# Optimization experiments

Measured on AMD Instinct MI355X. Metric: run time of the kernel, lower is better.

Reference implementation:

```python
import jax, jax.numpy as jnp
import numpy as np

N_NODES = 8192
N_EDGES = 65536


def _segment_softmax(scores, seg_ids, num_segments):
    # scores: [E, 1], seg_ids: [E] -> softmax over edges sharing the same dst
    m = jax.ops.segment_max(scores, seg_ids, num_segments=num_segments)  # [N,1]
    e = jnp.exp(scores - m[seg_ids])
    denom = jax.ops.segment_sum(e, seg_ids, num_segments=num_segments)   # [N,1]
    return e / denom[seg_ids]


def setup_inputs() -> dict:
    key = jax.random.key(0)
    ks = jax.random.split(key, 12)
    s = lambda fin: 1.0 / np.sqrt(fin)
    inp = {
        'n_f': jax.random.normal(ks[0], (N_NODES, 1024), jnp.float32),
        'word2vec': jax.random.normal(ks[1], (N_NODES, 300), jnp.float32),
        's_f': jax.random.normal(ks[2], (N_EDGES, 16), jnp.float32),
        'src': jax.random.randint(ks[3], (N_EDGES,), 0, N_NODES),
        'dst': jax.random.randint(ks[4], (N_EDGES,), 0, N_NODES),
        'We': jax.random.normal(ks[5], (2064, 1024), jnp.float32) * s(2064),
        'be': jnp.zeros((1024,), jnp.float32),
        'Wel': jax.random.normal(ks[6], (600, 600), jnp.float32) * s(600),
        'bel': jnp.zeros((600,), jnp.float32),
        'Wa': jax.random.normal(ks[7], (1024, 1), jnp.float32) * s(1024),
        'ba': jnp.zeros((1,), jnp.float32),
        'Wal': jax.random.normal(ks[8], (600, 1), jnp.float32) * s(600),
        'bal': jnp.zeros((1,), jnp.float32),
        'Wn': jax.random.normal(ks[9], (2048, 1024), jnp.float32) * s(2048),
        'bn': jnp.zeros((1024,), jnp.float32),
        'Wnl': jax.random.normal(ks[10], (600, 300), jnp.float32) * s(600),
        'bnl': jnp.zeros((300,), jnp.float32),
    }
    return inp


def reference(n_f, word2vec, s_f, src, dst,
              We, be, Wel, bel, Wa, ba, Wal, bal, Wn, bn, Wnl, bnl):
    # ---- edge apply (H_H_EdgeApplyModule) ----
    src_nf = n_f[src]                                    # [E,1024] gather
    feat = jnp.concatenate([src_nf, s_f, n_f[dst]], axis=1)  # [E,2064]
    e_f = jax.nn.relu(feat @ We + be)                    # [E,1024]
    feat_lang = jnp.concatenate([word2vec[src], word2vec[dst]], axis=1)  # [E,600]
    e_f_lang = jax.nn.relu(feat_lang @ Wel + bel)        # [E,600]

    # ---- edge attention (E_AttentionModule1): scalar score per edge ----
    a_feat = e_f @ Wa + ba                               # [E,1]
    a_feat_lang = e_f_lang @ Wal + bal                   # [E,1]

    # ---- reduce: mailbox softmax over incoming edges per dst node ----
    alpha = _segment_softmax(a_feat, dst, N_NODES)       # [E,1]
    alpha_lang = _segment_softmax(a_feat_lang, dst, N_NODES)
    z_f = jax.ops.segment_sum(alpha * (src_nf + e_f), dst, num_segments=N_NODES)      # [N,1024]
    z_f_lang = jax.ops.segment_sum(alpha_lang * word2vec[src], dst, num_segments=N_NODES)  # [N,300]

    # ---- node apply (H_NodeApplyModule) ----
    new_n_f = jax.nn.relu(jnp.concatenate([n_f, z_f], axis=1) @ Wn + bn)              # [N,1024]
    new_n_f_lang = jax.nn.relu(jnp.concatenate([word2vec, z_f_lang], axis=1) @ Wnl + bnl)  # [N,300]
    return new_n_f, new_n_f_lang
```

## Files before the change

### kernel.cpp

```cpp
#include <hip/hip_runtime.h>
#include <hip/hip_bf16.h>

#define N_NODES 8192
#define N_EDGES 65536
#define OUT0_ELEMS ((size_t)N_NODES * 1024)

using bf16 = __hip_bfloat16;
typedef __attribute__((ext_vector_type(8))) short short8;
typedef __attribute__((ext_vector_type(4))) float f32x4;

__device__ __forceinline__ float b2f(bf16 x) { return __bfloat162float(x); }
__device__ __forceinline__ bf16 f2b(float x) { return __float2bfloat16(x); }
__device__ __forceinline__ unsigned short bbits(float x)
{
  union { bf16 h; unsigned short u; } v; v.h = f2b(x); return v.u;
}
__device__ __forceinline__ unsigned pack2(float a, float b)
{
  return (unsigned)bbits(a) | ((unsigned)bbits(b) << 16);
}
__device__ __forceinline__ float4 cvt2x(uint2 u)
{
  float4 r;
  r.x = __uint_as_float(u.x << 16);
  r.y = __uint_as_float(u.x & 0xffff0000u);
  r.z = __uint_as_float(u.y << 16);
  r.w = __uint_as_float(u.y & 0xffff0000u);
  return r;
}
__device__ __forceinline__ float4 ld4b(const bf16* p)
{
  uint2 u = *(const uint2*)p;
  return cvt2x(u);
}
__device__ __forceinline__ void st4b(bf16* p, float a, float b, float c, float d)
{
  uint2 v; v.x = pack2(a, b); v.y = pack2(c, d);
  *(uint2*)p = v;
}

__global__ void GNN_27650999451833_kernel() {}

__global__ void gnn6_zero(int* __restrict__ p, int n)
{
  int i = blockIdx.x * blockDim.x + threadIdx.x;
  if (i < n) p[i] = 0;
}

__global__ __launch_bounds__(256)
void gnn7_cvt(const float* __restrict__ src, bf16* __restrict__ dst, int n8)
{
  int i = blockIdx.x * blockDim.x + threadIdx.x;
  if (i < n8) {
    float4 a = ((const float4*)src)[2 * i];
    float4 b = ((const float4*)src)[2 * i + 1];
    uint4 p;
    p.x = pack2(a.x, a.y); p.y = pack2(a.z, a.w);
    p.z = pack2(b.x, b.y); p.w = pack2(b.z, b.w);
    ((uint4*)dst)[i] = p;
  }
}

__global__ __launch_bounds__(256)
void gnn8_pad_w2v(const float* __restrict__ src, bf16* __restrict__ dst)
{
  int idx = blockIdx.x * blockDim.x + threadIdx.x;
  if (idx >= N_NODES * 80) return;
  int r = idx / 80, c0 = (idx % 80) * 4;
  float v[4];
#pragma unroll
  for (int j = 0; j < 4; ++j) {
    int c = c0 + j;
    v[j] = (c < 300) ? src[(size_t)r * 300 + c] : 0.f;
  }
  uint2 p; p.x = pack2(v[0], v[1]); p.y = pack2(v[2], v[3]);
  *(uint2*)(dst + (size_t)r * 320 + c0) = p;
}

__global__ __launch_bounds__(256)
void gnn12_t_Wetail(const float* __restrict__ We, bf16* __restrict__ BT)
{
  int c = blockIdx.x * 256 + threadIdx.x;
  if (c >= 1024) return;
  bf16* row = BT + (size_t)c * 32;
#pragma unroll
  for (int k = 0; k < 16; ++k)
    row[k] = f2b(We[(size_t)(1024 + k) * 1024 + c]);
#pragma unroll
  for (int k = 16; k < 32; ++k) row[k] = f2b(0.f);
}

__global__ __launch_bounds__(256)
void gnn10_t_We(const float* __restrict__ src, bf16* __restrict__ dst)
{
  __shared__ float tile[32][33];
  const int kb = blockIdx.x * 32, nb = blockIdx.y * 32;
  const int tx = threadIdx.x & 31, ty = threadIdx.x >> 5;
  const int n = nb + tx;
#pragma unroll
  for (int i = ty; i < 32; i += 8)
    tile[i][tx] = (n < 1024)
        ? src[(size_t)(kb + i) * 1024 + n]
        : src[(size_t)(1040 + kb + i) * 1024 + (n - 1024)];
  __syncthreads();
#pragma unroll
  for (int i = ty; i < 32; i += 8)
    dst[(size_t)(nb + i) * 1024 + kb + tx] = f2b(tile[tx][i]);
}

__global__ __launch_bounds__(256)
void gnn10_t_Wn(const float* __restrict__ src, bf16* __restrict__ dst)
{
  __shared__ float tile[32][33];
  const int kb = blockIdx.x * 32, nb = blockIdx.y * 32;
  const int tx = threadIdx.x & 31, ty = threadIdx.x >> 5;
#pragma unroll
  for (int i = ty; i < 32; i += 8)
    tile[i][tx] = src[(size_t)(kb + i) * 1024 + nb + tx];
  __syncthreads();
#pragma unroll
  for (int i = ty; i < 32; i += 8)
    dst[(size_t)(nb + i) * 2048 + kb + tx] = f2b(tile[tx][i]);
}

__global__ __launch_bounds__(256)
void gnn10_t_Wel(const float* __restrict__ src, bf16* __restrict__ dst)
{
  __shared__ float tile[32][33];
  const int kb = blockIdx.x * 32, nb = blockIdx.y * 32;
  const int tx = threadIdx.x & 31, ty = threadIdx.x >> 5;
  const int n = nb + tx;
#pragma unroll
  for (int i = ty; i < 32; i += 8) {
    int k = kb + i;
    float v = 0.f;
    if (k < 300) {
      if (n < 600)       v = src[(size_t)k * 600 + n];
      else if (n < 1200) v = src[(size_t)(300 + k) * 600 + (n - 600)];
    }
    tile[i][tx] = v;
  }
  __syncthreads();
#pragma unroll
  for (int i = ty; i < 32; i += 8)
    dst[(size_t)(nb + i) * 320 + kb + tx] = f2b(tile[tx][i]);
}

__global__ __launch_bounds__(256)
void gnn10_t_Wnl(const float* __restrict__ src, bf16* __restrict__ dst)
{
  __shared__ float tile[32][33];
  const int kb = blockIdx.x * 32, nb = blockIdx.y * 32;
  const int tx = threadIdx.x & 31, ty = threadIdx.x >> 5;
  const int n = nb + tx;
#pragma unroll
  for (int i = ty; i < 32; i += 8) {
    int k = kb + i;
    int kr = (k < 300) ? k : ((k >= 320 && k < 620) ? (k - 20) : -1);
    tile[i][tx] = (kr >= 0 && n < 300) ? src[(size_t)kr * 300 + n] : 0.f;
  }
  __syncthreads();
#pragma unroll
  for (int i = ty; i < 32; i += 8)
    dst[(size_t)(nb + i) * 640 + kb + tx] = f2b(tile[tx][i]);
}

__global__ __launch_bounds__(256)
void gnn10_mm_P(const bf16* __restrict__ A, const bf16* __restrict__ BT,
                bf16* __restrict__ P, const float* __restrict__ be)
{
  __shared__ short As[128 * 40];
  __shared__ short Bs[128 * 40];
  const int t = threadIdx.x;
  const int col0 = blockIdx.x * 128, row0 = blockIdx.y * 128;
  const int lane = t & 63, w = t >> 6, m16 = lane & 15, q = lane >> 4;
  const int wr = w >> 1, wc = w & 1;

  f32x4 acc[4][4];
#pragma unroll
  for (int mi = 0; mi < 4; ++mi)
#pragma unroll
    for (int ni = 0; ni < 4; ++ni) acc[mi][ni] = (f32x4){0.f, 0.f, 0.f, 0.f};

  const int ar = t >> 1, ah = (t & 1) * 16;
  const bf16* aptr = A + (size_t)(row0 + ar) * 1024 + ah;
  const bf16* bptr = BT + (size_t)(col0 + ar) * 1024 + ah;

  uint4 a0 = *(const uint4*)(aptr);
  uint4 a1 = *(const uint4*)(aptr + 8);
  uint4 b0 = *(const uint4*)(bptr);
  uint4 b1 = *(const uint4*)(bptr + 8);

  for (int k0 = 0; k0 < 1024; k0 += 32) {
    if (k0) __syncthreads();
    *(uint4*)&As[ar * 40 + ah] = a0;
    *(uint4*)&As[ar * 40 + ah + 8] = a1;
    *(uint4*)&Bs[ar * 40 + ah] = b0;
    *(uint4*)&Bs[ar * 40 + ah + 8] = b1;
    __syncthreads();
    if (k0 + 32 < 1024) {
      a0 = *(const uint4*)(aptr + k0 + 32);
      a1 = *(const uint4*)(aptr + k0 + 40);
      b0 = *(const uint4*)(bptr + k0 + 32);
      b1 = *(const uint4*)(bptr + k0 + 40);
    }
    short8 af[4];
#pragma unroll
    for (int mi = 0; mi < 4; ++mi)
      af[mi] = *(const short8*)&As[(wr * 64 + mi * 16 + m16) * 40 + 8 * q];
#pragma unroll
    for (int ni = 0; ni < 4; ++ni) {
      short8 bfv = *(const short8*)&Bs[(wc * 64 + ni * 16 + m16) * 40 + 8 * q];
#pragma unroll
      for (int mi = 0; mi < 4; ++mi)
        acc[mi][ni] =
            __builtin_amdgcn_mfma_f32_16x16x32_bf16(af[mi], bfv, acc[mi][ni], 0, 0, 0);
    }
  }
#pragma unroll
  for (int mi = 0; mi < 4; ++mi)
#pragma unroll
    for (int ni = 0; ni < 4; ++ni) {
      int c = col0 + wc * 64 + ni * 16 + m16;
      float bias = (be != nullptr && c >= 1024) ? be[c - 1024] : 0.f;
#pragma unroll
      for (int r = 0; r < 4; ++r)
        P[(size_t)(row0 + wr * 64 + mi * 16 + 4 * q + r) * 2048 + c] =
            f2b(acc[mi][ni][r] + bias);
    }
}

__global__ __launch_bounds__(256)
void gnn10_mm_out_n(const bf16* __restrict__ A0, const bf16* __restrict__ A1,
                    const bf16* __restrict__ BT, const float* __restrict__ bn,
                    float* __restrict__ out)
{
  __shared__ short As[128 * 40];
  __shared__ short Bs[128 * 40];
  const int t = threadIdx.x;
  const int col0 = blockIdx.x * 128, row0 = blockIdx.y * 128;
  const int lane = t & 63, w = t >> 6, m16 = lane & 15, q = lane >> 4;
  const int wr = w >> 1, wc = w & 1;

  f32x4 acc[4][4];
#pragma unroll
  for (int mi = 0; mi < 4; ++mi)
#pragma unroll
    for (int ni = 0; ni < 4; ++ni) acc[mi][ni] = (f32x4){0.f, 0.f, 0.f, 0.f};

  const int ar = t >> 1, ah = (t & 1) * 16;
  const bf16* ap0 = A0 + (size_t)(row0 + ar) * 1024 + ah;
  const bf16* ap1 = A1 + (size_t)(row0 + ar) * 1024 + ah;
  const bf16* bptr = BT + (size_t)(col0 + ar) * 2048 + ah;

  uint4 a0 = *(const uint4*)(ap0);
  uint4 a1 = *(const uint4*)(ap0 + 8);
  uint4 b0 = *(const uint4*)(bptr);
  uint4 b1 = *(const uint4*)(bptr + 8);

  for (int k0 = 0; k0 < 2048; k0 += 32) {
    if (k0) __syncthreads();
    *(uint4*)&As[ar * 40 + ah] = a0;
    *(uint4*)&As[ar * 40 + ah + 8] = a1;
    *(uint4*)&Bs[ar * 40 + ah] = b0;
    *(uint4*)&Bs[ar * 40 + ah + 8] = b1;
    __syncthreads();
    if (k0 + 32 < 2048) {
      int kn = k0 + 32;
      const bf16* ap = (kn < 1024) ? (ap0 + kn) : (ap1 + (kn - 1024));
      a0 = *(const uint4*)(ap);
      a1 = *(const uint4*)(ap + 8);
      b0 = *(const uint4*)(bptr + kn);
      b1 = *(const uint4*)(bptr + kn + 8);
    }
    short8 af[4];
#pragma unroll
    for (int mi = 0; mi < 4; ++mi)
      af[mi] = *(const short8*)&As[(wr * 64 + mi * 16 + m16) * 40 + 8 * q];
#pragma unroll
    for (int ni = 0; ni < 4; ++ni) {
      short8 bfv = *(const short8*)&Bs[(wc * 64 + ni * 16 + m16) * 40 + 8 * q];
#pragma unroll
      for (int mi = 0; mi < 4; ++mi)
        acc[mi][ni] =
            __builtin_amdgcn_mfma_f32_16x16x32_bf16(af[mi], bfv, acc[mi][ni], 0, 0, 0);
    }
  }
#pragma unroll
  for (int mi = 0; mi < 4; ++mi)
#pragma unroll
    for (int ni = 0; ni < 4; ++ni) {
      int c = col0 + wc * 64 + ni * 16 + m16;
      float bias = bn[c];
#pragma unroll
      for (int r = 0; r < 4; ++r) {
        float v = acc[mi][ni][r] + bias;
        out[(size_t)(row0 + wr * 64 + mi * 16 + 4 * q + r) * 1024 + c] =
            fmaxf(v, 0.f);
      }
    }
}

__global__ __launch_bounds__(256)
void gnn10_mm_Q(const bf16* __restrict__ A, const bf16* __restrict__ BT,
                bf16* __restrict__ Q, const float* __restrict__ bel)
{
  __shared__ short As[128 * 40];
  __shared__ short Bs[128 * 40];
  const int t = threadIdx.x;
  const int col0 = blockIdx.x * 128, row0 = blockIdx.y * 128;
  const int lane = t & 63, w = t >> 6, m16 = lane & 15, q = lane >> 4;
  const int wr = w >> 1, wc = w & 1;

  f32x4 acc[4][4];
#pragma unroll
  for (int mi = 0; mi < 4; ++mi)
#pragma unroll
    for (int ni = 0; ni < 4; ++ni) acc[mi][ni] = (f32x4){0.f, 0.f, 0.f, 0.f};

  const int ar = t >> 1, ah = (t & 1) * 16;
  const bf16* aptr = A + (size_t)(row0 + ar) * 320 + ah;
  const bf16* bptr = BT + (size_t)(col0 + ar) * 320 + ah;

  uint4 a0 = *(const uint4*)(aptr);
  uint4 a1 = *(const uint4*)(aptr + 8);
  uint4 b0 = *(const uint4*)(bptr);
  uint4 b1 = *(const uint4*)(bptr + 8);

  for (int k0 = 0; k0 < 320; k0 += 32) {
    if (k0) __syncthreads();
    *(uint4*)&As[ar * 40 + ah] = a0;
    *(uint4*)&As[ar * 40 + ah + 8] = a1;
    *(uint4*)&Bs[ar * 40 + ah] = b0;
    *(uint4*)&Bs[ar * 40 + ah + 8] = b1;
    __syncthreads();
    if (k0 + 32 < 320) {
      a0 = *(const uint4*)(aptr + k0 + 32);
      a1 = *(const uint4*)(aptr + k0 + 40);
      b0 = *(const uint4*)(bptr + k0 + 32);
      b1 = *(const uint4*)(bptr + k0 + 40);
    }
    short8 af[4];
#pragma unroll
    for (int mi = 0; mi < 4; ++mi)
      af[mi] = *(const short8*)&As[(wr * 64 + mi * 16 + m16) * 40 + 8 * q];
#pragma unroll
    for (int ni = 0; ni < 4; ++ni) {
      short8 bfv = *(const short8*)&Bs[(wc * 64 + ni * 16 + m16) * 40 + 8 * q];
#pragma unroll
      for (int mi = 0; mi < 4; ++mi)
        acc[mi][ni] =
            __builtin_amdgcn_mfma_f32_16x16x32_bf16(af[mi], bfv, acc[mi][ni], 0, 0, 0);
    }
  }
#pragma unroll
  for (int mi = 0; mi < 4; ++mi)
#pragma unroll
    for (int ni = 0; ni < 4; ++ni) {
      int c = col0 + wc * 64 + ni * 16 + m16;
      float bias = (bel != nullptr && c >= 600 && c < 1200) ? bel[c - 600] : 0.f;
#pragma unroll
      for (int r = 0; r < 4; ++r)
        Q[(size_t)(row0 + wr * 64 + mi * 16 + 4 * q + r) * 1280 + c] =
            f2b(acc[mi][ni][r] + bias);
    }
}

__global__ __launch_bounds__(256)
void gnn10_mm_out_l(const bf16* __restrict__ A0, const bf16* __restrict__ A1,
                    const bf16* __restrict__ BT, const float* __restrict__ bnl,
                    float* __restrict__ out2)
{
  __shared__ short As[128 * 40];
  __shared__ short Bs[128 * 40];
  const int t = threadIdx.x;
  const int col0 = blockIdx.x * 128, row0 = blockIdx.y * 128;
  const int lane = t & 63, w = t >> 6, m16 = lane & 15, q = lane >> 4;
  const int wr = w >> 1, wc = w & 1;

  f32x4 acc[4][4];
#pragma unroll
  for (int mi = 0; mi < 4; ++mi)
#pragma unroll
    for (int ni = 0; ni < 4; ++ni) acc[mi][ni] = (f32x4){0.f, 0.f, 0.f, 0.f};

  const int ar = t >> 1, ah = (t & 1) * 16;
  const bf16* ap0 = A0 + (size_t)(row0 + ar) * 320 + ah;
  const bf16* ap1 = A1 + (size_t)(row0 + ar) * 320 + ah;
  const bf16* bptr = BT + (size_t)(col0 + ar) * 640 + ah;

  uint4 a0 = *(const uint4*)(ap0);
  uint4 a1 = *(const uint4*)(ap0 + 8);
  uint4 b0 = *(const uint4*)(bptr);
  uint4 b1 = *(const uint4*)(bptr + 8);

  for (int k0 = 0; k0 < 640; k0 += 32) {
    if (k0) __syncthreads();
    *(uint4*)&As[ar * 40 + ah] = a0;
    *(uint4*)&As[ar * 40 + ah + 8] = a1;
    *(uint4*)&Bs[ar * 40 + ah] = b0;
    *(uint4*)&Bs[ar * 40 + ah + 8] = b1;
    __syncthreads();
    if (k0 + 32 < 640) {
      int kn = k0 + 32;
      const bf16* ap = (kn < 320) ? (ap0 + kn) : (ap1 + (kn - 320));
      a0 = *(const uint4*)(ap);
      a1 = *(const uint4*)(ap + 8);
      b0 = *(const uint4*)(bptr + kn);
      b1 = *(const uint4*)(bptr + kn + 8);
    }
    short8 af[4];
#pragma unroll
    for (int mi = 0; mi < 4; ++mi)
      af[mi] = *(const short8*)&As[(wr * 64 + mi * 16 + m16) * 40 + 8 * q];
#pragma unroll
    for (int ni = 0; ni < 4; ++ni) {
      short8 bfv = *(const short8*)&Bs[(wc * 64 + ni * 16 + m16) * 40 + 8 * q];
#pragma unroll
      for (int mi = 0; mi < 4; ++mi)
        acc[mi][ni] =
            __builtin_amdgcn_mfma_f32_16x16x32_bf16(af[mi], bfv, acc[mi][ni], 0, 0, 0);
    }
  }
#pragma unroll
  for (int mi = 0; mi < 4; ++mi)
#pragma unroll
    for (int ni = 0; ni < 4; ++ni) {
      int c = col0 + wc * 64 + ni * 16 + m16;
      if (c < 300) {
        float bias = bnl[c];
#pragma unroll
        for (int r = 0; r < 4; ++r) {
          float v = acc[mi][ni][r] + bias;
          out2[(size_t)(row0 + wr * 64 + mi * 16 + 4 * q + r) * 300 + c] =
              fmaxf(v, 0.f);
        }
      }
    }
}

__global__ void gnn6_count(const int* __restrict__ dst, int* __restrict__ cnt)
{
  int e = blockIdx.x * blockDim.x + threadIdx.x;
  if (e < N_EDGES) atomicAdd(&cnt[dst[e]], 1);
}

__global__ __launch_bounds__(1024)
void gnn6_scan(const int* __restrict__ cnt, int* __restrict__ off, int* __restrict__ cur)
{
  __shared__ int sh[1024];
  const int t = threadIdx.x;
  int local[8]; int sum = 0;
#pragma unroll
  for (int i = 0; i < 8; ++i) { int v = cnt[t * 8 + i]; local[i] = sum; sum += v; }
  sh[t] = sum;
  __syncthreads();
  for (int d = 1; d < 1024; d <<= 1) {
    int v = (t >= d) ? sh[t - d] : 0;
    __syncthreads();
    sh[t] += v;
    __syncthreads();
  }
  int basev = (t > 0) ? sh[t - 1] : 0;
#pragma unroll
  for (int i = 0; i < 8; ++i) { int o = basev + local[i]; off[t * 8 + i] = o; cur[t * 8 + i] = o; }
  if (t == 1023) off[8192] = sh[1023];
}

__global__ void gnn6_fill(const int* __restrict__ dst, int* __restrict__ cur,
                          int* __restrict__ elist)
{
  int e = blockIdx.x * blockDim.x + threadIdx.x;
  if (e < N_EDGES) { int p = atomicAdd(&cur[dst[e]], 1); elist[p] = e; }
}

__global__ void gnn14_fill(const int* __restrict__ dst, const int* __restrict__ src,
                           int* __restrict__ cur, int* __restrict__ elist,
                           int* __restrict__ srcs, int* __restrict__ dsts)
{
  int e = blockIdx.x * blockDim.x + threadIdx.x;
  if (e < N_EDGES) {
    int d = dst[e];
    int p = atomicAdd(&cur[d], 1);
    elist[p] = e;
    srcs[p] = src[e];
    dsts[p] = d;
  }
}

__global__ __launch_bounds__(256)
void gnn14_sfp(const float* __restrict__ s_f, const int* __restrict__ elist,
               bf16* __restrict__ sfp)
{
  int p = blockIdx.x * 256 + threadIdx.x;
  if (p >= N_EDGES) return;
  int e = elist[p];
  const float4* sp = (const float4*)(s_f + (size_t)e * 16);
  float4 s0 = sp[0], s1 = sp[1], s2 = sp[2], s3 = sp[3];
  uint4 lo, hi;
  lo.x = pack2(s0.x, s0.y); lo.y = pack2(s0.z, s0.w);
  lo.z = pack2(s1.x, s1.y); lo.w = pack2(s1.z, s1.w);
  hi.x = pack2(s2.x, s2.y); hi.y = pack2(s2.z, s2.w);
  hi.z = pack2(s3.x, s3.y); hi.w = pack2(s3.z, s3.w);
  uint4* dp = (uint4*)(sfp + (size_t)p * 32);
  dp[0] = lo; dp[1] = hi;
  dp[2] = (uint4){0, 0, 0, 0}; dp[3] = (uint4){0, 0, 0, 0};
}

#define SLD_STRIDE 1032
__global__ __launch_bounds__(256)
void gnn14_mm_S_score(const bf16* __restrict__ sfp, const bf16* __restrict__ WeTtail,
                      const int* __restrict__ srcs, const int* __restrict__ dsts,
                      const float* __restrict__ Wa, const float* __restrict__ ba,
                      const float* __restrict__ Wal, const float* __restrict__ bal,
                      const bf16* __restrict__ P, const bf16* __restrict__ Q,
                      bf16* __restrict__ S, float* __restrict__ af,
                      float* __restrict__ afl)
{
  __shared__ short Sld[16 * SLD_STRIDE];
  __shared__ float shf[8][4], shl[8][4];
  const int t = threadIdx.x;
  const int lane = t & 63, w = t >> 6, m16 = lane & 15, q = lane >> 4;
  const int p0 = blockIdx.x * 16;

  short8 bfr = *(const short8*)(sfp + (size_t)(p0 + m16) * 32 + 8 * q);
  const int cb = w * 256;
#pragma unroll
  for (int ni = 0; ni < 16; ++ni) {
    short8 afr = *(const short8*)(WeTtail + (size_t)(cb + ni * 16 + m16) * 32 + 8 * q);
    f32x4 acc = __builtin_amdgcn_mfma_f32_16x16x32_bf16(
        afr, bfr, (f32x4){0.f, 0.f, 0.f, 0.f}, 0, 0, 0);
    uint2 v; v.x = pack2(acc[0], acc[1]); v.y = pack2(acc[2], acc[3]);
    *(uint2*)&Sld[m16 * SLD_STRIDE + cb + ni * 16 + 4 * q] = v;
  }
  __syncthreads();

  {
    const int row = t >> 4, cbase = (t & 15) * 8;
#pragma unroll
    for (int j = 0; j < 8; ++j) {
      uint4 v = *(const uint4*)&Sld[row * SLD_STRIDE + cbase + 128 * j];
      *(uint4*)(S + (size_t)(p0 + row) * 1024 + cbase + 128 * j) = v;
    }
  }

  const int c0 = 4 * t;
  float4 wav = *(const float4*)(Wa + c0);
  const bool lact = (t < 150);
  float4 walv = {0, 0, 0, 0};
  if (lact) walv = *(const float4*)(Wal + c0);
  const float ba0 = ba[0], bal0 = bal[0];

#pragma unroll 1
  for (int bb = 0; bb < 2; ++bb) {
    const int eb = 8 * bb;
    int ss[8], dd[8];
    {
      int4 a4 = *(const int4*)(srcs + p0 + eb);
      int4 b4 = *(const int4*)(srcs + p0 + eb + 4);
      ss[0] = a4.x; ss[1] = a4.y; ss[2] = a4.z; ss[3] = a4.w;
      ss[4] = b4.x; ss[5] = b4.y; ss[6] = b4.z; ss[7] = b4.w;
      int4 c4 = *(const int4*)(dsts + p0 + eb);
      int4 d4 = *(const int4*)(dsts + p0 + eb + 4);
      dd[0] = c4.x; dd[1] = c4.y; dd[2] = c4.z; dd[3] = c4.w;
      dd[4] = d4.x; dd[5] = d4.y; dd[6] = d4.z; dd[7] = d4.w;
    }

    float pf[8], pl[8];
#pragma unroll
    for (int i = 0; i < 8; ++i) {
      uint2 us = *(const uint2*)&Sld[(eb + i) * SLD_STRIDE + c0];
      float4 sv = cvt2x(us);
      float4 p1 = ld4b(P + (size_t)ss[i] * 2048 + c0);
      float4 p2 = ld4b(P + (size_t)dd[i] * 2048 + 1024 + c0);
      float acc = 0.f;
      acc = fmaf(fmaxf(p1.x + p2.x + sv.x, 0.f), wav.x, acc);
      acc = fmaf(fmaxf(p1.y + p2.y + sv.y, 0.f), wav.y, acc);
      acc = fmaf(fmaxf(p1.z + p2.z + sv.z, 0.f), wav.z, acc);
      acc = fmaf(fmaxf(p1.w + p2.w + sv.w, 0.f), wav.w, acc);
      pf[i] = acc;

      float accl = 0.f;
      if (lact) {
        float4 q1 = ld4b(Q + (size_t)ss[i] * 1280 + c0);
        float4 q2 = ld4b(Q + (size_t)dd[i] * 1280 + 600 + c0);
        accl = fmaf(fmaxf(q1.x + q2.x, 0.f), walv.x, accl);
        accl = fmaf(fmaxf(q1.y + q2.y, 0.f), walv.y, accl);
        accl = fmaf(fmaxf(q1.z + q2.z, 0.f), walv.z, accl);
        accl = fmaf(fmaxf(q1.w + q2.w, 0.f), walv.w, accl);
      }
      pl[i] = accl;
    }

#pragma unroll
    for (int i = 0; i < 8; ++i) {
#pragma unroll
      for (int o = 32; o > 0; o >>= 1) {
        pf[i] += __shfl_down(pf[i], o, 64);
        pl[i] += __shfl_down(pl[i], o, 64);
      }
    }
    if (lane == 0) {
#pragma unroll
      for (int i = 0; i < 8; ++i) { shf[i][w] = pf[i]; shl[i][w] = pl[i]; }
    }
    __syncthreads();
    if (t < 8)
      af[p0 + eb + t] = shf[t][0] + shf[t][1] + shf[t][2] + shf[t][3] + ba0;
    if (t >= 64 && t < 72) {
      const int i = t & 7;
      afl[p0 + eb + i] = shl[i][0] + shl[i][1] + shl[i][2] + shl[i][3] + bal0;
    }
    __syncthreads();
  }
}

__global__ __launch_bounds__(256)
void gnn11_edge_score(const int* __restrict__ src, const int* __restrict__ dst,
                      const float* __restrict__ s_f, const float* __restrict__ We,
                      const float* __restrict__ be, const float* __restrict__ Wa,
                      const float* __restrict__ ba, const float* __restrict__ bel,
                      const float* __restrict__ Wal, const float* __restrict__ bal,
                      const bf16* __restrict__ P, const bf16* __restrict__ Q,
                      float* __restrict__ af, float* __restrict__ afl)
{
  const int t = threadIdx.x;
  const int lane = t & 63, w = t >> 6;
  const int c0 = 4 * t;
  const int e0 = blockIdx.x * 8;

  float wef[16][4];
#pragma unroll
  for (int k = 0; k < 16; ++k) {
    float4 v = *(const float4*)(We + (size_t)(1024 + k) * 1024 + c0);
    wef[k][0] = v.x; wef[k][1] = v.y; wef[k][2] = v.z; wef[k][3] = v.w;
  }
  float4 bev = *(const float4*)(be + c0);
  float4 wav = *(const float4*)(Wa + c0);
  const bool lact = (t < 150);
  float4 belv = {0, 0, 0, 0}, walv = {0, 0, 0, 0};
  if (lact) { belv = *(const float4*)(bel + c0); walv = *(const float4*)(Wal + c0); }

  int ss[8], dd[8];
  {
    int4 a = *(const int4*)(src + e0);
    int4 b = *(const int4*)(src + e0 + 4);
    ss[0] = a.x; ss[1] = a.y; ss[2] = a.z; ss[3] = a.w;
    ss[4] = b.x; ss[5] = b.y; ss[6] = b.z; ss[7] = b.w;
    int4 c = *(const int4*)(dst + e0);
    int4 d = *(const int4*)(dst + e0 + 4);
    dd[0] = c.x; dd[1] = c.y; dd[2] = c.z; dd[3] = c.w;
    dd[4] = d.x; dd[5] = d.y; dd[6] = d.z; dd[7] = d.w;
  }

  float pf[8], pl[8];

#pragma unroll
  for (int i = 0; i < 8; ++i) {
    const int e = e0 + i;
    float sfv[16];
    {
      const float4* sp = (const float4*)(s_f + (size_t)e * 16);
      float4 s0 = sp[0], s1 = sp[1], s2 = sp[2], s3 = sp[3];
      sfv[0] = s0.x; sfv[1] = s0.y; sfv[2] = s0.z; sfv[3] = s0.w;
      sfv[4] = s1.x; sfv[5] = s1.y; sfv[6] = s1.z; sfv[7] = s1.w;
      sfv[8] = s2.x; sfv[9] = s2.y; sfv[10] = s2.z; sfv[11] = s2.w;
      sfv[12] = s3.x; sfv[13] = s3.y; sfv[14] = s3.z; sfv[15] = s3.w;
    }
    float4 p1 = ld4b(P + (size_t)ss[i] * 2048 + c0);
    float4 p2 = ld4b(P + (size_t)dd[i] * 2048 + 1024 + c0);
    float pv[4] = {p1.x + p2.x + bev.x, p1.y + p2.y + bev.y,
                   p1.z + p2.z + bev.z, p1.w + p2.w + bev.w};
    float acc = 0.f;
#pragma unroll
    for (int j = 0; j < 4; ++j) {
      float v = pv[j];
#pragma unroll
      for (int k = 0; k < 16; ++k) v = fmaf(sfv[k], wef[k][j], v);
      acc = fmaf(fmaxf(v, 0.f), (&wav.x)[j], acc);
    }
    pf[i] = acc;

    float accl = 0.f;
    if (lact) {
      float4 q1 = ld4b(Q + (size_t)ss[i] * 1280 + c0);
      float4 q2 = ld4b(Q + (size_t)dd[i] * 1280 + 600 + c0);
      float qv[4] = {q1.x + q2.x + belv.x, q1.y + q2.y + belv.y,
                     q1.z + q2.z + belv.z, q1.w + q2.w + belv.w};
#pragma unroll
      for (int j = 0; j < 4; ++j)
        accl = fmaf(fmaxf(qv[j], 0.f), (&walv.x)[j], accl);
    }
    pl[i] = accl;
  }

  __shared__ float shf[8][4], shl[8][4];
#pragma unroll
  for (int i = 0; i < 8; ++i) {
#pragma unroll
    for (int o = 32; o > 0; o >>= 1) {
      pf[i] += __shfl_down(pf[i], o, 64);
      pl[i] += __shfl_down(pl[i], o, 64);
    }
  }
  if (lane == 0) {
#pragma unroll
    for (int i = 0; i < 8; ++i) { shf[i][w] = pf[i]; shl[i][w] = pl[i]; }
  }
  __syncthreads();
  if (t < 8)
    af[e0 + t] = shf[t][0] + shf[t][1] + shf[t][2] + shf[t][3] + ba[0];
  if (t >= 64 && t < 72) {
    const int i = t & 7;
    afl[e0 + i] = shl[i][0] + shl[i][1] + shl[i][2] + shl[i][3] + bal[0];
  }
}

__global__ __launch_bounds__(256)
void gnn14_alpha(const int* __restrict__ off, float* __restrict__ af,
                 float* __restrict__ afl)
{
  const int n = blockIdx.x * 256 + threadIdx.x;
  if (n >= N_NODES) return;
  const int base = off[n];
  const int deg = off[n + 1] - base;
  float m = -1e30f, ml = -1e30f;
  for (int i = 0; i < deg; ++i) {
    m = fmaxf(m, af[base + i]);
    ml = fmaxf(ml, afl[base + i]);
  }
  float den = 0.f, denl = 0.f;
  for (int i = 0; i < deg; ++i) {
    den += expf(af[base + i] - m);
    denl += expf(afl[base + i] - ml);
  }
  float inv = (den > 0.f) ? 1.f / den : 0.f;
  float invl = (denl > 0.f) ? 1.f / denl : 0.f;
  for (int i = 0; i < deg; ++i) {
    af[base + i] = expf(af[base + i] - m) * inv;
    afl[base + i] = expf(afl[base + i] - ml) * invl;
  }
}

__global__ __launch_bounds__(256)
void gnn6_alpha(const int* __restrict__ off, const int* __restrict__ elist,
                float* __restrict__ af, float* __restrict__ afl)
{
  const int n = blockIdx.x * 256 + threadIdx.x;
  if (n >= N_NODES) return;
  const int base = off[n];
  const int deg = off[n + 1] - base;
  float m = -1e30f, ml = -1e30f;
  for (int i = 0; i < deg; ++i) {
    int e = elist[base + i];
    m = fmaxf(m, af[e]);
    ml = fmaxf(ml, afl[e]);
  }
  float den = 0.f, denl = 0.f;
  for (int i = 0; i < deg; ++i) {
    int e = elist[base + i];
    den += expf(af[e] - m);
    denl += expf(afl[e] - ml);
  }
  float inv = (den > 0.f) ? 1.f / den : 0.f;
  float invl = (denl > 0.f) ? 1.f / denl : 0.f;
  for (int i = 0; i < deg; ++i) {
    int e = elist[base + i];
    af[e] = expf(af[e] - m) * inv;
    afl[e] = expf(afl[e] - ml) * invl;
  }
}

__global__ __launch_bounds__(256)
void gnn14_node_z(const int* __restrict__ off, const int* __restrict__ srcs,
                  const float* __restrict__ af, const float* __restrict__ afl,
                  const bf16* __restrict__ nf_bf, const bf16* __restrict__ w2v_pad,
                  const bf16* __restrict__ S, const bf16* __restrict__ P,
                  bf16* __restrict__ zf, bf16* __restrict__ zfl_pad)
{
  const int node = blockIdx.x;
  const int t = threadIdx.x;
  const int c0 = 4 * t;
  const int base = off[node];
  const int deg = off[node + 1] - base;

  float4 p2v = ld4b(P + (size_t)node * 2048 + 1024 + c0);
  const float p2[4] = {p2v.x, p2v.y, p2v.z, p2v.w};

  float acc[4] = {0.f, 0.f, 0.f, 0.f};
  float accl[4] = {0.f, 0.f, 0.f, 0.f};
  const bool lact = (t < 75);

  for (int i = 0; i < deg; ++i) {
    const int pidx = base + i;
    const int s = srcs[pidx];
    const float wgt = af[pidx];
    const float wl = afl[pidx];

    float4 sv = ld4b(S + (size_t)pidx * 1024 + c0);
    float4 p1 = ld4b(P + (size_t)s * 2048 + c0);
    float4 nf4 = ld4b(nf_bf + (size_t)s * 1024 + c0);
    const float p1a[4] = {p1.x, p1.y, p1.z, p1.w};
    const float sva[4] = {sv.x, sv.y, sv.z, sv.w};
    const float nfa[4] = {nf4.x, nf4.y, nf4.z, nf4.w};
#pragma unroll
    for (int j = 0; j < 4; ++j) {
      float ef = fmaxf(p1a[j] + p2[j] + sva[j], 0.f);
      acc[j] = fmaf(wgt, nfa[j] + ef, acc[j]);
    }
    if (lact) {
      float4 wv = ld4b(w2v_pad + (size_t)s * 320 + c0);
      accl[0] = fmaf(wl, wv.x, accl[0]);
      accl[1] = fmaf(wl, wv.y, accl[1]);
      accl[2] = fmaf(wl, wv.z, accl[2]);
      accl[3] = fmaf(wl, wv.w, accl[3]);
    }
  }
  st4b(zf + (size_t)node * 1024 + c0, acc[0], acc[1], acc[2], acc[3]);
  if (lact)
    st4b(zfl_pad + (size_t)node * 320 + c0, accl[0], accl[1], accl[2], accl[3]);
  else if (t < 80)
    st4b(zfl_pad + (size_t)node * 320 + c0, 0.f, 0.f, 0.f, 0.f);
}

__global__ __launch_bounds__(256)
void gnn9_node_z(const int* __restrict__ off, const int* __restrict__ elist,
                 const int* __restrict__ src, const float* __restrict__ af,
                 const float* __restrict__ afl, const bf16* __restrict__ nf_bf,
                 const bf16* __restrict__ w2v_pad, const float* __restrict__ s_f,
                 const float* __restrict__ We, const float* __restrict__ be,
                 const bf16* __restrict__ P, bf16* __restrict__ zf,
                 bf16* __restrict__ zfl_pad)
{
  const int node = blockIdx.x;
  const int t = threadIdx.x;
  const int c0 = 4 * t;
  const int base = off[node];
  const int deg = off[node + 1] - base;

  float wef[16][4];
#pragma unroll
  for (int k = 0; k < 16; ++k) {
    float4 v = *(const float4*)(We + (size_t)(1024 + k) * 1024 + c0);
    wef[k][0] = v.x; wef[k][1] = v.y; wef[k][2] = v.z; wef[k][3] = v.w;
  }
  float4 p2v = ld4b(P + (size_t)node * 2048 + 1024 + c0);
  float4 bev = *(const float4*)(be + c0);
  const float p2[4] = {p2v.x + bev.x, p2v.y + bev.y, p2v.z + bev.z, p2v.w + bev.w};

  float acc[4] = {0.f, 0.f, 0.f, 0.f};
  float accl[4] = {0.f, 0.f, 0.f, 0.f};
  const bool lact = (t < 75);

  for (int i = 0; i < deg; ++i) {
    const int e = elist[base + i];
    const int s = src[e];
    const float wgt = af[e];
    const float wl = afl[e];

    float sfv[16];
    {
      const float4* sp = (const float4*)(s_f + (size_t)e * 16);
      float4 s0 = sp[0], s1 = sp[1], s2 = sp[2], s3 = sp[3];
      sfv[0] = s0.x; sfv[1] = s0.y; sfv[2] = s0.z; sfv[3] = s0.w;
      sfv[4] = s1.x; sfv[5] = s1.y; sfv[6] = s1.z; sfv[7] = s1.w;
      sfv[8] = s2.x; sfv[9] = s2.y; sfv[10] = s2.z; sfv[11] = s2.w;
      sfv[12] = s3.x; sfv[13] = s3.y; sfv[14] = s3.z; sfv[15] = s3.w;
    }

    float4 p1 = ld4b(P + (size_t)s * 2048 + c0);
    float4 nf4 = ld4b(nf_bf + (size_t)s * 1024 + c0);
    const float p1a[4] = {p1.x, p1.y, p1.z, p1.w};
    const float nfa[4] = {nf4.x, nf4.y, nf4.z, nf4.w};
#pragma unroll
    for (int j = 0; j < 4; ++j) {
      float ef = p1a[j] + p2[j];
#pragma unroll
      for (int k = 0; k < 16; ++k) ef = fmaf(sfv[k], wef[k][j], ef);
      ef = fmaxf(ef, 0.f);
      acc[j] = fmaf(wgt, nfa[j] + ef, acc[j]);
    }
    if (lact) {
      float4 wv = ld4b(w2v_pad + (size_t)s * 320 + c0);
      accl[0] = fmaf(wl, wv.x, accl[0]);
      accl[1] = fmaf(wl, wv.y, accl[1]);
      accl[2] = fmaf(wl, wv.z, accl[2]);
      accl[3] = fmaf(wl, wv.w, accl[3]);
    }
  }
  st4b(zf + (size_t)node * 1024 + c0, acc[0], acc[1], acc[2], acc[3]);
  if (lact)
    st4b(zfl_pad + (size_t)node * 320 + c0, accl[0], accl[1], accl[2], accl[3]);
  else if (t < 80)
    st4b(zfl_pad + (size_t)node * 320 + c0, 0.f, 0.f, 0.f, 0.f);
}

extern "C" void kernel_launch(void* const* d_in, const int* in_sizes, int n_in,
                              void* d_out, int out_size, void* d_ws, size_t ws_size,
                              hipStream_t stream)
{
  (void)hipGetLastError();
  if (n_in != 17) { (void)hipMemsetAsync(d_out, 0x41, 4096, stream); return; }

  const float* n_f = (const float*)d_in[0];
  const float* w2v = (const float*)d_in[1];
  const float* s_f = (const float*)d_in[2];
  const int*   src = (const int*)d_in[3];
  const int*   dst = (const int*)d_in[4];
  const float* We  = (const float*)d_in[5];
  const float* be  = (const float*)d_in[6];
  const float* Wel = (const float*)d_in[7];
  const float* bel = (const float*)d_in[8];
  const float* Wa  = (const float*)d_in[9];
  const float* ba  = (const float*)d_in[10];
  const float* Wal = (const float*)d_in[11];
  const float* bal = (const float*)d_in[12];
  const float* Wn  = (const float*)d_in[13];
  const float* bn  = (const float*)d_in[14];
  const float* Wnl = (const float*)d_in[15];
  const float* bnl = (const float*)d_in[16];
  float* out  = (float*)d_out;
  float* out2 = out + OUT0_ELEMS;

  char* ws = (char*)d_ws;
  size_t o = 0;
  auto alloc = [&](size_t bytes) -> void* {
    void* p = ws + o; o += bytes; o = (o + 255) & ~(size_t)255; return p;
  };
  bf16* P        = (bf16*)alloc((size_t)N_NODES * 2048 * 2);
  bf16* Q        = (bf16*)alloc((size_t)N_NODES * 1280 * 2);
  bf16* zf       = (bf16*)alloc((size_t)N_NODES * 1024 * 2);
  bf16* zfl_pad  = (bf16*)alloc((size_t)N_NODES * 320 * 2);
  bf16* nf_bf    = (bf16*)alloc((size_t)N_NODES * 1024 * 2);
  bf16* w2v_pad  = (bf16*)alloc((size_t)N_NODES * 320 * 2);
  bf16* WeT      = (bf16*)alloc((size_t)2048 * 1024 * 2);
  bf16* WnT      = (bf16*)alloc((size_t)1024 * 2048 * 2);
  bf16* WelT     = (bf16*)alloc((size_t)1280 * 320 * 2);
  bf16* WnlT     = (bf16*)alloc((size_t)384 * 640 * 2);
  float* af      = (float*)alloc((size_t)N_EDGES * 4);
  float* afl     = (float*)alloc((size_t)N_EDGES * 4);
  int* cnt       = (int*)alloc((size_t)N_NODES * 4);
  int* offs      = (int*)alloc((size_t)(N_NODES + 1) * 4);
  int* cur       = (int*)alloc((size_t)N_NODES * 4);
  int* elist     = (int*)alloc((size_t)N_EDGES * 4);
  size_t base_end = o;
  if (base_end > ws_size) { (void)hipMemsetAsync(d_out, 0x42, 4096, stream); return; }

  bf16* sfp     = (bf16*)alloc((size_t)N_EDGES * 32 * 2);
  bf16* WeTtail = (bf16*)alloc((size_t)1024 * 32 * 2);
  bf16* S       = (bf16*)alloc((size_t)N_EDGES * 1024 * 2);
  int* srcs     = (int*)alloc((size_t)N_EDGES * 4);
  int* dsts     = (int*)alloc((size_t)N_EDGES * 4);
  const bool useS = (o <= ws_size);

  gnn6_zero<<<N_NODES / 256, 256, 0, stream>>>(cnt, N_NODES);
  gnn7_cvt<<<(N_NODES * 1024 / 8 + 255) / 256, 256, 0, stream>>>(n_f, nf_bf,
                                                                 N_NODES * 1024 / 8);
  gnn8_pad_w2v<<<(N_NODES * 80 + 255) / 256, 256, 0, stream>>>(w2v, w2v_pad);
  { dim3 g(32, 64); gnn10_t_We<<<g, 256, 0, stream>>>(We, WeT); }
  { dim3 g(64, 32); gnn10_t_Wn<<<g, 256, 0, stream>>>(Wn, WnT); }
  { dim3 g(10, 40); gnn10_t_Wel<<<g, 256, 0, stream>>>(Wel, WelT); }
  { dim3 g(20, 12); gnn10_t_Wnl<<<g, 256, 0, stream>>>(Wnl, WnlT); }

  gnn6_count<<<N_EDGES / 256, 256, 0, stream>>>(dst, cnt);
  gnn6_scan<<<1, 1024, 0, stream>>>(cnt, offs, cur);
  if (useS) {
    gnn14_fill<<<N_EDGES / 256, 256, 0, stream>>>(dst, src, cur, elist, srcs, dsts);
    gnn12_t_Wetail<<<4, 256, 0, stream>>>(We, WeTtail);
    gnn14_sfp<<<N_EDGES / 256, 256, 0, stream>>>(s_f, elist, sfp);
  } else {
    gnn6_fill<<<N_EDGES / 256, 256, 0, stream>>>(dst, cur, elist);
  }

  {
    dim3 g(2048 / 128, N_NODES / 128);
    gnn10_mm_P<<<g, 256, 0, stream>>>(nf_bf, WeT, P, useS ? be : nullptr);
  }
  {
    dim3 g(1280 / 128, N_NODES / 128);
    gnn10_mm_Q<<<g, 256, 0, stream>>>(w2v_pad, WelT, Q, useS ? bel : nullptr);
  }

  if (useS) {
    gnn14_mm_S_score<<<N_EDGES / 16, 256, 0, stream>>>(
        sfp, WeTtail, srcs, dsts, Wa, ba, Wal, bal, P, Q, S, af, afl);
    gnn14_alpha<<<N_NODES / 256, 256, 0, stream>>>(offs, af, afl);
    gnn14_node_z<<<N_NODES, 256, 0, stream>>>(offs, srcs, af, afl, nf_bf,
                                              w2v_pad, S, P, zf, zfl_pad);
  } else {
    gnn11_edge_score<<<N_EDGES / 8, 256, 0, stream>>>(src, dst, s_f, We, be, Wa,
                                                      ba, bel, Wal, bal, P, Q,
                                                      af, afl);
    gnn6_alpha<<<N_NODES / 256, 256, 0, stream>>>(offs, elist, af, afl);
    gnn9_node_z<<<N_NODES, 256, 0, stream>>>(offs, elist, src, af, afl, nf_bf,
                                             w2v_pad, s_f, We, be, P, zf, zfl_pad);
  }

  {
    dim3 g(1024 / 128, N_NODES / 128);
    gnn10_mm_out_n<<<g, 256, 0, stream>>>(nf_bf, zf, WnT, bn, out);
  }
  {
    dim3 g(384 / 128, N_NODES / 128);
    gnn10_mm_out_l<<<g, 256, 0, stream>>>(w2v_pad, zfl_pad, WnlT, bnl, out2);
  }

  if (hipGetLastError() != hipSuccess) (void)hipMemsetAsync(d_out, 0x44, 4096, stream);
}
```

Before: 480.4 us.

## Recompute s_f projection in node_z instead of storing edge S buffer

Drops the materialized per-edge S tensor (E x 1024 bf16), which was written by the score kernel and read back by node_z. Both kernels now recompute the small s_f @ We_tail projection with MFMA into shared memory. The score kernel handles 8 edges per block, and node_z processes incoming edges in chunks of 8. This removes about 256 MB of global write plus read traffic. In exchange it duplicates MFMA work, leaves half of each 16-row MFMA unused, and adds block syncs per chunk in node_z.

```diff
diff --git a/kernel.cpp b/kernel.cpp
--- a/kernel.cpp
+++ b/kernel.cpp
@@ -507,111 +507,98 @@
   dp[2] = (uint4){0, 0, 0, 0}; dp[3] = (uint4){0, 0, 0, 0};
 }
 
-#define SLD_STRIDE 1032
-__global__ __launch_bounds__(256)
-void gnn14_mm_S_score(const bf16* __restrict__ sfp, const bf16* __restrict__ WeTtail,
-                      const int* __restrict__ srcs, const int* __restrict__ dsts,
-                      const float* __restrict__ Wa, const float* __restrict__ ba,
-                      const float* __restrict__ Wal, const float* __restrict__ bal,
-                      const bf16* __restrict__ P, const bf16* __restrict__ Q,
-                      bf16* __restrict__ S, float* __restrict__ af,
-                      float* __restrict__ afl)
-{
-  __shared__ short Sld[16 * SLD_STRIDE];
+#define SLDS 1032
+__global__ __launch_bounds__(256)
+void gnn15_score(const bf16* __restrict__ sfp, const bf16* __restrict__ WeTtail,
+                 const int* __restrict__ srcs, const int* __restrict__ dsts,
+                 const float* __restrict__ Wa, const float* __restrict__ ba,
+                 const float* __restrict__ Wal, const float* __restrict__ bal,
+                 const bf16* __restrict__ P, const bf16* __restrict__ Q,
+                 float* __restrict__ af, float* __restrict__ afl)
+{
+  __shared__ short Sld[8 * SLDS];
   __shared__ float shf[8][4], shl[8][4];
   const int t = threadIdx.x;
   const int lane = t & 63, w = t >> 6, m16 = lane & 15, q = lane >> 4;
-  const int p0 = blockIdx.x * 16;
-
-  short8 bfr = *(const short8*)(sfp + (size_t)(p0 + m16) * 32 + 8 * q);
+  const int p0 = blockIdx.x * 8;
+
+  const int brow = p0 + (m16 < 8 ? m16 : 7);
+  short8 bfr = *(const short8*)(sfp + (size_t)brow * 32 + 8 * q);
   const int cb = w * 256;
 #pragma unroll
   for (int ni = 0; ni < 16; ++ni) {
     short8 afr = *(const short8*)(WeTtail + (size_t)(cb + ni * 16 + m16) * 32 + 8 * q);
     f32x4 acc = __builtin_amdgcn_mfma_f32_16x16x32_bf16(
         afr, bfr, (f32x4){0.f, 0.f, 0.f, 0.f}, 0, 0, 0);
-    uint2 v; v.x = pack2(acc[0], acc[1]); v.y = pack2(acc[2], acc[3]);
-    *(uint2*)&Sld[m16 * SLD_STRIDE + cb + ni * 16 + 4 * q] = v;
+    if (m16 < 8) {
+      uint2 v; v.x = pack2(acc[0], acc[1]); v.y = pack2(acc[2], acc[3]);
+      *(uint2*)&Sld[m16 * SLDS + cb + ni * 16 + 4 * q] = v;
+    }
   }
   __syncthreads();
-
-  {
-    const int row = t >> 4, cbase = (t & 15) * 8;
-#pragma unroll
-    for (int j = 0; j < 8; ++j) {
-      uint4 v = *(const uint4*)&Sld[row * SLD_STRIDE + cbase + 128 * j];
-      *(uint4*)(S + (size_t)(p0 + row) * 1024 + cbase + 128 * j) = v;
-    }
-  }
 
   const int c0 = 4 * t;
   float4 wav = *(const float4*)(Wa + c0);
   const bool lact = (t < 150);
   float4 walv = {0, 0, 0, 0};
   if (lact) walv = *(const float4*)(Wal + c0);
-  const float ba0 = ba[0], bal0 = bal[0];
-
-#pragma unroll 1
-  for (int bb = 0; bb < 2; ++bb) {
-    const int eb = 8 * bb;
-    int ss[8], dd[8];
-    {
-      int4 a4 = *(const int4*)(srcs + p0 + eb);
-      int4 b4 = *(const int4*)(srcs + p0 + eb + 4);
-      ss[0] = a4.x; ss[1] = a4.y; ss[2] = a4.z; ss[3] = a4.w;
-      ss[4] = b4.x; ss[5] = b4.y; ss[6] = b4.z; ss[7] = b4.w;
-      int4 c4 = *(const int4*)(dsts + p0 + eb);
-      int4 d4 = *(const int4*)(dsts + p0 + eb + 4);
-      dd[0] = c4.x; dd[1] = c4.y; dd[2] = c4.z; dd[3] = c4.w;
-      dd[4] = d4.x; dd[5] = d4.y; dd[6] = d4.z; dd[7] = d4.w;
-    }
-
-    float pf[8], pl[8];
-#pragma unroll
-    for (int i = 0; i < 8; ++i) {
-      uint2 us = *(const uint2*)&Sld[(eb + i) * SLD_STRIDE + c0];
-      float4 sv = cvt2x(us);
-      float4 p1 = ld4b(P + (size_t)ss[i] * 2048 + c0);
-      float4 p2 = ld4b(P + (size_t)dd[i] * 2048 + 1024 + c0);
-      float acc = 0.f;
-      acc = fmaf(fmaxf(p1.x + p2.x + sv.x, 0.f), wav.x, acc);
-      acc = fmaf(fmaxf(p1.y + p2.y + sv.y, 0.f), wav.y, acc);
-      acc = fmaf(fmaxf(p1.z + p2.z + sv.z, 0.f), wav.z, acc);
-      acc = fmaf(fmaxf(p1.w + p2.w + sv.w, 0.f), wav.w, acc);
-      pf[i] = acc;
-
-      float accl = 0.f;
-      if (lact) {
-        float4 q1 = ld4b(Q + (size_t)ss[i] * 1280 + c0);
-        float4 q2 = ld4b(Q + (size_t)dd[i] * 1280 + 600 + c0);
-        accl = fmaf(fmaxf(q1.x + q2.x, 0.f), walv.x, accl);
-        accl = fmaf(fmaxf(q1.y + q2.y, 0.f), walv.y, accl);
-        accl = fmaf(fmaxf(q1.z + q2.z, 0.f), walv.z, accl);
-        accl = fmaf(fmaxf(q1.w + q2.w, 0.f), walv.w, accl);
-      }
-      pl[i] = accl;
-    }
-
-#pragma unroll
-    for (int i = 0; i < 8; ++i) {
-#pragma unroll
-      for (int o = 32; o > 0; o >>= 1) {
-        pf[i] += __shfl_down(pf[i], o, 64);
-        pl[i] += __shfl_down(pl[i], o, 64);
-      }
-    }
-    if (lane == 0) {
-#pragma unroll
-      for (int i = 0; i < 8; ++i) { shf[i][w] = pf[i]; shl[i][w] = pl[i]; }
-    }
-    __syncthreads();
-    if (t < 8)
-      af[p0 + eb + t] = shf[t][0] + shf[t][1] + shf[t][2] + shf[t][3] + ba0;
-    if (t >= 64 && t < 72) {
-      const int i = t & 7;
-      afl[p0 + eb + i] = shl[i][0] + shl[i][1] + shl[i][2] + shl[i][3] + bal0;
-    }
-    __syncthreads();
+
+  int ss[8], dd[8];
+  {
+    int4 a4 = *(const int4*)(srcs + p0);
+    int4 b4 = *(const int4*)(srcs + p0 + 4);
+    ss[0] = a4.x; ss[1] = a4.y; ss[2] = a4.z; ss[3] = a4.w;
+    ss[4] = b4.x; ss[5] = b4.y; ss[6] = b4.z; ss[7] = b4.w;
+    int4 c4 = *(const int4*)(dsts + p0);
+    int4 d4 = *(const int4*)(dsts + p0 + 4);
+    dd[0] = c4.x; dd[1] = c4.y; dd[2] = c4.z; dd[3] = c4.w;
+    dd[4] = d4.x; dd[5] = d4.y; dd[6] = d4.z; dd[7] = d4.w;
+  }
+
+  float pf[8], pl[8];
+#pragma unroll
+  for (int i = 0; i < 8; ++i) {
+    uint2 us = *(const uint2*)&Sld[i * SLDS + c0];
+    float4 sv = cvt2x(us);
+    float4 p1 = ld4b(P + (size_t)ss[i] * 2048 + c0);
+    float4 p2 = ld4b(P + (size_t)dd[i] * 2048 + 1024 + c0);
+    float acc = 0.f;
+    acc = fmaf(fmaxf(p1.x + p2.x + sv.x, 0.f), wav.x, acc);
+    acc = fmaf(fmaxf(p1.y + p2.y + sv.y, 0.f), wav.y, acc);
+    acc = fmaf(fmaxf(p1.z + p2.z + sv.z, 0.f), wav.z, acc);
+    acc = fmaf(fmaxf(p1.w + p2.w + sv.w, 0.f), wav.w, acc);
+    pf[i] = acc;
+
+    float accl = 0.f;
+    if (lact) {
+      float4 q1 = ld4b(Q + (size_t)ss[i] * 1280 + c0);
+      float4 q2 = ld4b(Q + (size_t)dd[i] * 1280 + 600 + c0);
+      accl = fmaf(fmaxf(q1.x + q2.x, 0.f), walv.x, accl);
+      accl = fmaf(fmaxf(q1.y + q2.y, 0.f), walv.y, accl);
+      accl = fmaf(fmaxf(q1.z + q2.z, 0.f), walv.z, accl);
+      accl = fmaf(fmaxf(q1.w + q2.w, 0.f), walv.w, accl);
+    }
+    pl[i] = accl;
+  }
+
+#pragma unroll
+  for (int i = 0; i < 8; ++i) {
+#pragma unroll
+    for (int o = 32; o > 0; o >>= 1) {
+      pf[i] += __shfl_down(pf[i], o, 64);
+      pl[i] += __shfl_down(pl[i], o, 64);
+    }
+  }
+  if (lane == 0) {
+#pragma unroll
+    for (int i = 0; i < 8; ++i) { shf[i][w] = pf[i]; shl[i][w] = pl[i]; }
+  }
+  __syncthreads();
+  if (t < 8)
+    af[p0 + t] = shf[t][0] + shf[t][1] + shf[t][2] + shf[t][3] + ba[0];
+  if (t >= 64 && t < 72) {
+    const int i = t & 7;
+    afl[p0 + i] = shl[i][0] + shl[i][1] + shl[i][2] + shl[i][3] + bal[0];
   }
 }
 
@@ -772,14 +759,17 @@
 }
 
 __global__ __launch_bounds__(256)
-void gnn14_node_z(const int* __restrict__ off, const int* __restrict__ srcs,
+void gnn15_node_z(const int* __restrict__ off, const int* __restrict__ srcs,
                   const float* __restrict__ af, const float* __restrict__ afl,
                   const bf16* __restrict__ nf_bf, const bf16* __restrict__ w2v_pad,
-                  const bf16* __restrict__ S, const bf16* __restrict__ P,
-                  bf16* __restrict__ zf, bf16* __restrict__ zfl_pad)
-{
+                  const bf16* __restrict__ sfp, const bf16* __restrict__ WeTtail,
+                  const bf16* __restrict__ P, bf16* __restrict__ zf,
+                  bf16* __restrict__ zfl_pad)
+{
+  __shared__ short Sld[8 * SLDS];
   const int node = blockIdx.x;
   const int t = threadIdx.x;
+  const int lane = t & 63, w = t >> 6, m16 = lane & 15, q = lane >> 4;
   const int c0 = 4 * t;
   const int base = off[node];
   const int deg = off[node + 1] - base;
@@ -790,31 +780,53 @@
   float acc[4] = {0.f, 0.f, 0.f, 0.f};
   float accl[4] = {0.f, 0.f, 0.f, 0.f};
   const bool lact = (t < 75);
-
-  for (int i = 0; i < deg; ++i) {
-    const int pidx = base + i;
-    const int s = srcs[pidx];
-    const float wgt = af[pidx];
-    const float wl = afl[pidx];
-
-    float4 sv = ld4b(S + (size_t)pidx * 1024 + c0);
-    float4 p1 = ld4b(P + (size_t)s * 2048 + c0);
-    float4 nf4 = ld4b(nf_bf + (size_t)s * 1024 + c0);
-    const float p1a[4] = {p1.x, p1.y, p1.z, p1.w};
-    const float sva[4] = {sv.x, sv.y, sv.z, sv.w};
-    const float nfa[4] = {nf4.x, nf4.y, nf4.z, nf4.w};
-#pragma unroll
-    for (int j = 0; j < 4; ++j) {
-      float ef = fmaxf(p1a[j] + p2[j] + sva[j], 0.f);
-      acc[j] = fmaf(wgt, nfa[j] + ef, acc[j]);
-    }
-    if (lact) {
-      float4 wv = ld4b(w2v_pad + (size_t)s * 320 + c0);
-      accl[0] = fmaf(wl, wv.x, accl[0]);
-      accl[1] = fmaf(wl, wv.y, accl[1]);
-      accl[2] = fmaf(wl, wv.z, accl[2]);
-      accl[3] = fmaf(wl, wv.w, accl[3]);
-    }
+  const int cb = w * 256;
+
+  for (int ch = 0; ch < deg; ch += 8) {
+    const int p0 = base + ch;
+    int brow = p0 + (m16 < 8 ? m16 : 7);
+    if (brow > N_EDGES - 1) brow = N_EDGES - 1;
+    short8 bfr = *(const short8*)(sfp + (size_t)brow * 32 + 8 * q);
+#pragma unroll
+    for (int ni = 0; ni < 16; ++ni) {
+      short8 afr = *(const short8*)(WeTtail + (size_t)(cb + ni * 16 + m16) * 32 + 8 * q);
+      f32x4 sc = __builtin_amdgcn_mfma_f32_16x16x32_bf16(
+          afr, bfr, (f32x4){0.f, 0.f, 0.f, 0.f}, 0, 0, 0);
+      if (m16 < 8) {
+        uint2 v; v.x = pack2(sc[0], sc[1]); v.y = pack2(sc[2], sc[3]);
+        *(uint2*)&Sld[m16 * SLDS + cb + ni * 16 + 4 * q] = v;
+      }
+    }
+    __syncthreads();
+
+    const int iend = (deg < ch + 8) ? deg : (ch + 8);
+    for (int i = ch; i < iend; ++i) {
+      const int pidx = base + i;
+      const int s = srcs[pidx];
+      const float wgt = af[pidx];
+      const float wl = afl[pidx];
+
+      uint2 us = *(const uint2*)&Sld[(i - ch) * SLDS + c0];
+      float4 sv = cvt2x(us);
+      float4 p1 = ld4b(P + (size_t)s * 2048 + c0);
+      float4 nf4 = ld4b(nf_bf + (size_t)s * 1024 + c0);
+      const float p1a[4] = {p1.x, p1.y, p1.z, p1.w};
+      const float sva[4] = {sv.x, sv.y, sv.z, sv.w};
+      const float nfa[4] = {nf4.x, nf4.y, nf4.z, nf4.w};
+#pragma unroll
+      for (int j = 0; j < 4; ++j) {
+        float ef = fmaxf(p1a[j] + p2[j] + sva[j], 0.f);
+        acc[j] = fmaf(wgt, nfa[j] + ef, acc[j]);
+      }
+      if (lact) {
+        float4 wv = ld4b(w2v_pad + (size_t)s * 320 + c0);
+        accl[0] = fmaf(wl, wv.x, accl[0]);
+        accl[1] = fmaf(wl, wv.y, accl[1]);
+        accl[2] = fmaf(wl, wv.z, accl[2]);
+        accl[3] = fmaf(wl, wv.w, accl[3]);
+      }
+    }
+    __syncthreads();
   }
   st4b(zf + (size_t)node * 1024 + c0, acc[0], acc[1], acc[2], acc[3]);
   if (lact)
@@ -948,7 +960,6 @@
 
   bf16* sfp     = (bf16*)alloc((size_t)N_EDGES * 32 * 2);
   bf16* WeTtail = (bf16*)alloc((size_t)1024 * 32 * 2);
-  bf16* S       = (bf16*)alloc((size_t)N_EDGES * 1024 * 2);
   int* srcs     = (int*)alloc((size_t)N_EDGES * 4);
   int* dsts     = (int*)alloc((size_t)N_EDGES * 4);
   const bool useS = (o <= ws_size);
@@ -982,11 +993,12 @@
   }
 
   if (useS) {
-    gnn14_mm_S_score<<<N_EDGES / 16, 256, 0, stream>>>(
-        sfp, WeTtail, srcs, dsts, Wa, ba, Wal, bal, P, Q, S, af, afl);
+    gnn15_score<<<N_EDGES / 8, 256, 0, stream>>>(
+        sfp, WeTtail, srcs, dsts, Wa, ba, Wal, bal, P, Q, af, afl);
     gnn14_alpha<<<N_NODES / 256, 256, 0, stream>>>(offs, af, afl);
-    gnn14_node_z<<<N_NODES, 256, 0, stream>>>(offs, srcs, af, afl, nf_bf,
-                                              w2v_pad, S, P, zf, zfl_pad);
+    gnn15_node_z<<<N_NODES, 256, 0, stream>>>(offs, srcs, af, afl, nf_bf,
+                                              w2v_pad, sfp, WeTtail, P, zf,
+                                              zfl_pad);
   } else {
     gnn11_edge_score<<<N_EDGES / 8, 256, 0, stream>>>(src, dst, s_f, We, be, Wa,
                                                       ba, bel, Wal, bal, P, Q,
```

Result: slower. 492.1 us (+2.4%).
